# Kernel optimization log

Hardware: AMD Instinct MI355X
Metric: run time of the kernel (lower is better)

Reference implementation:

```python
import jax, jax.numpy as jnp
import numpy as np

B, N_REL, N_OBJ, N_ATT, VOCAB, D = 32, 1024, 1024, 4, 2048, 512


def setup_inputs() -> dict:
    key = jax.random.key(0)
    ks = jax.random.split(key, 12)
    inp = {}
    inp["ssg_rel"] = jax.random.randint(ks[0], (B, N_REL, 3), 0, N_OBJ, dtype=jnp.int32)
    inp["ssg_obj"] = jax.random.randint(ks[1], (B, N_OBJ), 0, VOCAB, dtype=jnp.int32)
    inp["ssg_att"] = jax.random.randint(ks[2], (B, N_OBJ, N_ATT), 0, VOCAB, dtype=jnp.int32)
    inp["emb_table"] = jax.random.normal(ks[3], (VOCAB, D), jnp.float32) * 0.02
    def lin(k, fan_in):
        return jax.random.normal(k, (fan_in, D), jnp.float32) * (1.0 / np.sqrt(fan_in))
    inp["W_sbj"] = lin(ks[4], 3 * D); inp["b_sbj"] = jnp.zeros((D,), jnp.float32)
    inp["W_obj"] = lin(ks[5], 3 * D); inp["b_obj"] = jnp.zeros((D,), jnp.float32)
    inp["W_rel"] = lin(ks[6], 3 * D); inp["b_rel"] = jnp.zeros((D,), jnp.float32)
    inp["W_o"] = lin(ks[7], D);      inp["b_o"] = jnp.zeros((D,), jnp.float32)
    inp["W_a"] = lin(ks[8], 2 * D);  inp["b_a"] = jnp.zeros((D,), jnp.float32)
    return inp


def reference(ssg_rel, ssg_obj, ssg_att, emb_table,
              W_sbj, b_sbj, W_obj, b_obj, W_rel, b_rel, W_o, b_o, W_a, b_a):
    # Dropout is identity in eval mode.
    Bq, N_rel, _ = ssg_rel.shape
    _, N_obj, N_att = ssg_att.shape
    d = emb_table.shape[1]

    rel_mask = (ssg_rel[:, :, 2] == 1)[..., None]      # [B, N_rel, 1], True = pad
    obj_mask = ssg_obj == 1                            # [B, N_obj]
    attr_mask = ssg_att == 1                           # [B, N_obj, N_att]

    rel_emb = emb_table[ssg_rel[:, :, 2]]              # [B, N_rel, d]
    obj_emb = emb_table[ssg_obj]                       # [B, N_obj, d]
    attr_emb = emb_table[ssg_att]                      # [B, N_obj, N_att, d]

    sbj_id = ssg_rel[:, :, 0]
    obj_id = ssg_rel[:, :, 1]
    gather = lambda ids: jnp.take_along_axis(obj_emb, ids[..., None], axis=1)  # [B,N_rel,d]
    sbj_g = gather(sbj_id)
    obj_g = gather(obj_id)

    zfill = lambda x: jnp.where(rel_mask, 0.0, x)
    # Sequential overwriting matches the original: rel_obj/rel_rel use the UPDATED sbj/obj feats.
    sbj_f = zfill(jax.nn.relu(jnp.concatenate([sbj_g, obj_g, rel_emb], -1) @ W_sbj + b_sbj))
    obj_f = zfill(jax.nn.relu(jnp.concatenate([sbj_f, obj_g, rel_emb], -1) @ W_obj + b_obj))
    rel_f = zfill(jax.nn.relu(jnp.concatenate([sbj_f, obj_f, rel_emb], -1) @ W_rel + b_rel))

    node = jnp.where(obj_mask[..., None], 0.0, jax.nn.relu(obj_emb @ W_o + b_o))  # [B,N_obj,d]

    att_in = jnp.concatenate(
        [jnp.broadcast_to(obj_emb[:, :, None, :], (Bq, N_obj, N_att, d)), attr_emb], -1)
    att_f = jnp.where(attr_mask[..., None], 0.0, jax.nn.relu(att_in @ W_a + b_a))  # [B,N_obj,N_att,d]

    bidx = jnp.arange(Bq)[:, None]
    node = node.at[bidx, sbj_id].add(sbj_f)
    node = node.at[bidx, obj_id].add(obj_f)

    # Original builds counts=ones(B, 2*N_rel, N_obj+1) then scatters 1s into it -> a no-op,
    # so counts.sum(dim=1) == 2*N_rel everywhere; the divisor is the constant 2*N_rel.
    rel_object_feat = node / jnp.asarray(2.0 * N_rel, node.dtype)

    att_sum = att_f.sum(axis=2)                        # [B, N_obj, d]
    att_cnt = jnp.sum(~attr_mask, axis=-1)             # [B, N_obj] number of valid attrs
    attr_zero = att_cnt == 0
    denom = jnp.maximum(att_cnt, 1).astype(att_sum.dtype)[..., None]
    att_feat = jnp.where(attr_zero[..., None], 0.0, att_sum / denom)

    ssg_feat = jnp.concatenate([rel_object_feat, rel_f, att_feat], axis=1)
    ssg_mask = jnp.concatenate([obj_mask, rel_mask[..., 0], attr_zero], axis=1)[:, None, None, :]
    return ssg_feat, ssg_mask
```

## Files before the change

### kernel.cpp

```cpp
#include <hip/hip_runtime.h>
#include <hip/hip_bf16.h>

typedef __attribute__((ext_vector_type(8))) short bf16x8;
typedef __attribute__((ext_vector_type(4))) float f32x4;

#define N_OBJ 1024
#define N_REL 1024
#define NB 32
#define D 512
#define VOCAB 2048
#define M_ROWS (NB * N_REL)
#define PRE_BLK (VOCAB * D)
#define WT_BLK (D * D)

__device__ __forceinline__ ushort f2bf(float f) {
    union { float f; unsigned u; } v; v.f = f;
    unsigned u = v.u;
    unsigned r = (u + 0x7FFFu + ((u >> 16) & 1u)) >> 16;
    return (ushort)r;
}
__device__ __forceinline__ float bf2f(ushort h) {
    union { unsigned u; float f; } v; v.u = ((unsigned)h) << 16;
    return v.f;
}

__device__ __forceinline__ void gload16(const ushort* g, const ushort* l) {
    __builtin_amdgcn_global_load_lds(
        (const __attribute__((address_space(1))) void*)(unsigned long long)(const void*)g,
        (__attribute__((address_space(3))) void*)(unsigned)(unsigned long long)(const void*)l,
        16, 0, 0);
}
__device__ __forceinline__ unsigned lds_off(const void* p) {
    return (unsigned)(unsigned long long)(const __attribute__((address_space(3))) void*)p;
}
__device__ __forceinline__ bf16x8 ds_read128(unsigned off) {
    bf16x8 r;
    asm volatile("ds_read_b128 %0, %1" : "=v"(r) : "v"(off));
    return r;
}

__device__ __forceinline__ void gemm0_body(
    int mt, int nt, int q, int tid,
    ushort* __restrict__ sA, ushort* __restrict__ sB,
    const ushort* __restrict__ A, const ushort* __restrict__ WT,
    ushort* __restrict__ PREB) {
    const int m0 = mt * 128;
    const int wtq[9] = {0, 1, 2, 4, 5, 8, 9, 10, 11};
    const ushort* BT0 = WT + (size_t)wtq[q] * WT_BLK + (size_t)nt * 128 * 512;
    ushort* PREq = PREB + (size_t)q * PRE_BLK;

    const int wave = tid >> 6;
    const int wm = wave >> 1, wn = wave & 1;
    const int lr = tid & 15, lk = (tid & 63) >> 4;

    f32x4 acc[4][4];
#pragma unroll
    for (int mi = 0; mi < 4; mi++)
#pragma unroll
        for (int ni = 0; ni < 4; ni++)
            acc[mi][ni] = (f32x4){0.f, 0.f, 0.f, 0.f};

    const ushort* Ag = A + (size_t)m0 * 512;
    const int srow = tid >> 3;
    const int scol = (tid & 7) * 8;

    for (int k0 = 0; k0 < 512; k0 += 64) {
        const ushort* As = Ag + (size_t)srow * 512 + k0 + scol;
        const ushort* Bs = BT0 + (size_t)srow * 512 + k0 + scol;
#pragma unroll
        for (int i = 0; i < 4; i++)
            gload16(As + (size_t)i * 32 * 512, &sA[i * 2048 + tid * 8]);
#pragma unroll
        for (int i = 0; i < 4; i++)
            gload16(Bs + (size_t)i * 32 * 512, &sB[i * 2048 + tid * 8]);
        __syncthreads();
#pragma unroll
        for (int ks = 0; ks < 2; ks++) {
            bf16x8 af[4], bfr[4];
#pragma unroll
            for (int mi = 0; mi < 4; mi++)
                af[mi] = *(const bf16x8*)&sA[(wm * 64 + mi * 16 + lr) * 64 + ks * 32 + lk * 8];
#pragma unroll
            for (int ni = 0; ni < 4; ni++)
                bfr[ni] = *(const bf16x8*)&sB[(wn * 64 + ni * 16 + lr) * 64 + ks * 32 + lk * 8];
#pragma unroll
            for (int mi = 0; mi < 4; mi++)
#pragma unroll
                for (int ni = 0; ni < 4; ni++)
                    acc[mi][ni] = __builtin_amdgcn_mfma_f32_16x16x32_bf16(af[mi], bfr[ni], acc[mi][ni], 0, 0, 0);
        }
        __syncthreads();
    }
#pragma unroll
    for (int mi = 0; mi < 4; mi++)
#pragma unroll
        for (int ni = 0; ni < 4; ni++) {
            int ch = nt * 128 + wn * 64 + ni * 16 + lr;
#pragma unroll
            for (int j = 0; j < 4; j++) {
                int R = m0 + wm * 64 + mi * 16 + lk * 4 + j;
                PREq[(size_t)R * 512 + ch] = f2bf(acc[mi][ni][j]);
            }
        }
}

template <int MODE>
__global__ __launch_bounds__(512, 2)
void k_gemm8(const ushort* __restrict__ A, const ushort* __restrict__ WT,
             const ushort* __restrict__ PREB,
             const int* __restrict__ ssg_rel, const int* __restrict__ ssg_obj,
             const float* __restrict__ bias,
             ushort* __restrict__ featbuf, float* __restrict__ out0,
             float* __restrict__ out1) {
    constexpr int KTOT = (MODE == 2) ? 1024 : 512;
    constexpr int NK = KTOT / 32;
    constexpr int LDA = 1024;
    __shared__ __attribute__((aligned(16))) ushort lds[4 * 2 * 256 * 32];

    const int tid = threadIdx.x;
    int x = blockIdx.x & 7, jj = blockIdx.x >> 3;
    const int mt = x * 16 + (jj >> 1), nt = jj & 1;
    const int m0 = mt * 256, n0 = nt * 256;

    const ushort* BT0 = WT + (size_t)((MODE == 1) ? 3 : 6) * WT_BLK + (size_t)n0 * 512;
    const ushort* BT1 = (MODE == 2) ? (WT + (size_t)7 * WT_BLK + (size_t)n0 * 512) : nullptr;

    const ushort* Ag = A + (size_t)m0 * LDA;
    const int srow = tid >> 2;
    const int scol = (tid & 3) * 8;

    const int wave = tid >> 6, lane = tid & 63;
    const int wm = wave >> 2, wn = wave & 3;
    const int lr = lane & 15, lk = lane >> 4;

    f32x4 acc[8][4];
#pragma unroll
    for (int mi = 0; mi < 8; mi++)
#pragma unroll
        for (int ni = 0; ni < 4; ni++)
            acc[mi][ni] = (f32x4){0.f, 0.f, 0.f, 0.f};

#define STAGE(KT) do {                                                          \
        int _b = (KT) & 3;                                                      \
        ushort* _dA = &lds[(_b * 2 + 0) * 8192];                                \
        ushort* _dB = &lds[(_b * 2 + 1) * 8192];                                \
        int _k0 = (KT) * 32;                                                    \
        const ushort* _Bb = (MODE == 2 && _k0 >= 512) ? (BT1 + (_k0 - 512))     \
                                                      : (BT0 + _k0);            \
        gload16(Ag + (size_t)(srow) * LDA + _k0 + scol, _dA + srow * 32 + scol);        \
        gload16(Ag + (size_t)(srow + 128) * LDA + _k0 + scol, _dA + (srow + 128) * 32 + scol); \
        gload16(_Bb + (size_t)(srow) * 512 + scol, _dB + srow * 32 + scol);             \
        gload16(_Bb + (size_t)(srow + 128) * 512 + scol, _dB + (srow + 128) * 32 + scol); \
    } while (0)

    STAGE(0); STAGE(1); STAGE(2);

    for (int kt = 0; kt < NK; ++kt) {
        if (kt + 3 < NK) {
            asm volatile("s_waitcnt vmcnt(8)\n\ts_barrier" ::: "memory");
            STAGE(kt + 3);
        } else if (kt + 3 == NK) {
            asm volatile("s_waitcnt vmcnt(8)\n\ts_barrier" ::: "memory");
        } else if (kt + 2 == NK) {
            asm volatile("s_waitcnt vmcnt(4)\n\ts_barrier" ::: "memory");
        } else {
            asm volatile("s_waitcnt vmcnt(0)\n\ts_barrier" ::: "memory");
        }
        {
            int buf = kt & 3;
            unsigned baseA = lds_off(&lds[(buf * 2 + 0) * 8192]) + (unsigned)(wm * 128) * 64 + lk * 16;
            unsigned baseB = lds_off(&lds[(buf * 2 + 1) * 8192]) + (unsigned)(wn * 64) * 64 + lk * 16;
            bf16x8 bfr[4], af[8];
#pragma unroll
            for (int ni = 0; ni < 4; ni++)
                bfr[ni] = ds_read128(baseB + (unsigned)(ni * 16 + lr) * 64);
#pragma unroll
            for (int mi = 0; mi < 8; mi++)
                af[mi] = ds_read128(baseA + (unsigned)(mi * 16 + lr) * 64);
            asm volatile("s_waitcnt lgkmcnt(0)" ::: "memory");
            __builtin_amdgcn_sched_barrier(0);
            __builtin_amdgcn_s_setprio(1);
#pragma unroll
            for (int mi = 0; mi < 8; mi++)
#pragma unroll
                for (int ni = 0; ni < 4; ni++)
                    acc[mi][ni] = __builtin_amdgcn_mfma_f32_16x16x32_bf16(af[mi], bfr[ni], acc[mi][ni], 0, 0, 0);
            __builtin_amdgcn_s_setprio(0);
        }
    }
#undef STAGE

    __syncthreads();
    int* sIo  = (int*)lds;
    int* sRid = sIo + 256;
    if (tid < 256) {
        int R = m0 + tid;
        int rid = ssg_rel[R * 3 + 2];
        sRid[tid] = rid;
        if (MODE == 1) sIo[tid] = ssg_obj[(R & ~(N_OBJ - 1)) + ssg_rel[R * 3 + 1]];
        if (MODE == 2 && nt == 0) {
            int b = R >> 10, rr = R & (N_REL - 1);
            out1[(size_t)b * 3072 + 1024 + rr] = (rid == 1) ? 1.0f : 0.0f;
        }
    }
    __syncthreads();

#pragma unroll
    for (int mi = 0; mi < 8; mi++) {
#pragma unroll
        for (int ni = 0; ni < 4; ni++) {
            int ch = n0 + wn * 64 + ni * 16 + lr;
#pragma unroll
            for (int j = 0; j < 4; j++) {
                int rl = wm * 128 + mi * 16 + lk * 4 + j;
                int R = m0 + rl;
                float v = acc[mi][ni][j];
                if (MODE == 1) {
                    int rid = sRid[rl];
                    int io = sIo[rl];
                    float t = v + bf2f(PREB[(size_t)3 * PRE_BLK + (size_t)io * 512 + ch])
                                + bf2f(PREB[(size_t)4 * PRE_BLK + (size_t)rid * 512 + ch])
                                + bias[ch];
                    t = fmaxf(t, 0.f);
                    if (rid == 1) t = 0.f;
                    featbuf[(size_t)R * 1024 + 512 + ch] = f2bf(t);
                } else {
                    int rid = sRid[rl];
                    float t = v + bf2f(PREB[(size_t)5 * PRE_BLK + (size_t)rid * 512 + ch])
                                + bias[ch];
                    t = fmaxf(t, 0.f);
                    if (rid == 1) t = 0.f;
                    int b = R >> 10, rr = R & (N_REL - 1);
                    out0[((size_t)(b * 3072 + 1024 + rr)) * 512 + ch] = t;
                }
            }
        }
    }
}

__global__ __launch_bounds__(256)
void k_setup(const float* __restrict__ E, ushort* __restrict__ EB,
             const float* __restrict__ Wsbj, const float* __restrict__ Wobj,
             const float* __restrict__ Wrel, const float* __restrict__ Wo,
             const float* __restrict__ Wa, ushort* __restrict__ WT,
             int* __restrict__ cnt) {
    int blk = blockIdx.x, tid = threadIdx.x;
    if (blk < 1024) {
        int i = blk * 256 + tid;
        float4 v = ((const float4*)E)[i];
        ushort4 o; o.x = f2bf(v.x); o.y = f2bf(v.y); o.z = f2bf(v.z); o.w = f2bf(v.w);
        ((ushort4*)EB)[i] = o;
    } else if (blk < 4096) {
        __shared__ float s[32][33];
        int bb = blk - 1024;
        int q = bb >> 8, rem = bb & 255;
        int bx = rem & 15, by = rem >> 4;
        const float* src; int ro;
        if (q < 3)       { src = Wsbj; ro = q * 512; }
        else if (q < 6)  { src = Wobj; ro = (q - 3) * 512; }
        else if (q < 9)  { src = Wrel; ro = (q - 6) * 512; }
        else if (q == 9) { src = Wo;   ro = 0; }
        else             { src = Wa;   ro = (q - 10) * 512; }
        int tx = tid & 31, ty = tid >> 5;
        int kbase = by * 32, nbase = bx * 32;
#pragma unroll
        for (int i = 0; i < 4; i++) {
            int k = kbase + ty + i * 8;
            s[ty + i * 8][tx] = src[(size_t)(ro + k) * 512 + nbase + tx];
        }
        __syncthreads();
        ushort* dst = WT + (size_t)q * WT_BLK;
#pragma unroll
        for (int i = 0; i < 4; i++) {
            int n = nbase + ty + i * 8;
            dst[(size_t)n * 512 + kbase + tx] = f2bf(s[tx][ty + i * 8]);
        }
    } else {
        cnt[(blk - 4096) * 256 + tid] = 0;
    }
}

__global__ void k_csr_count(const int* __restrict__ ssg_rel, int* __restrict__ cnt) {
    int r = blockIdx.x * 256 + threadIdx.x;
    int bb = r & ~(N_OBJ - 1);
    atomicAdd(&cnt[bb + ssg_rel[r * 3 + 0]], 1);
    atomicAdd(&cnt[bb + ssg_rel[r * 3 + 1]], 1);
}

__global__ __launch_bounds__(1024)
void k_csr_scan(const int* __restrict__ cnt, int* __restrict__ offs, int* __restrict__ cursor) {
    __shared__ int part[1024];
    int t = threadIdx.x;
    int base = t * 32;
    int local[32];
    int sum = 0;
#pragma unroll
    for (int i = 0; i < 32; i++) { local[i] = sum; sum += cnt[base + i]; }
    part[t] = sum;
    __syncthreads();
    for (int d = 1; d < 1024; d <<= 1) {
        int v = (t >= d) ? part[t - d] : 0;
        __syncthreads();
        part[t] += v;
        __syncthreads();
    }
    int excl = (t == 0) ? 0 : part[t - 1];
#pragma unroll
    for (int i = 0; i < 32; i++) {
        int o = excl + local[i];
        offs[base + i] = o;
        cursor[base + i] = o;
    }
    if (t == 1023) offs[32768] = part[1023];
}

__global__ __launch_bounds__(256)
void k_pre_fill(const ushort* __restrict__ EB, const ushort* __restrict__ WT,
                ushort* __restrict__ PREB, const int* __restrict__ ssg_rel,
                int* __restrict__ cursor, int* __restrict__ lists) {
    int blk = blockIdx.x, tid = threadIdx.x;
    if (blk < 576) {
        int q = blk >> 6, mt = (blk >> 2) & 15, nt = blk & 3;
        if ((q == 2 || q == 4 || q == 5) && mt >= 8) return;
        __shared__ __attribute__((aligned(16))) ushort sA[128 * 64];
        __shared__ __attribute__((aligned(16))) ushort sB[128 * 64];
        gemm0_body(mt, nt, q, tid, sA, sB, EB, WT, PREB);
    } else {
        int r = (blk - 576) * 256 + tid;
        int bb = r & ~(N_OBJ - 1);
        int p0 = atomicAdd(&cursor[bb + ssg_rel[r * 3 + 0]], 1);
        lists[p0] = r * 2;
        int p1 = atomicAdd(&cursor[bb + ssg_rel[r * 3 + 1]], 1);
        lists[p1] = r * 2 + 1;
    }
}

__global__ void k_sbj(const int* __restrict__ ssg_rel, const int* __restrict__ ssg_obj,
                      const ushort* __restrict__ PREB, const float* __restrict__ b_sbj,
                      ushort* __restrict__ featbuf) {
    int R = blockIdx.x * 2 + (threadIdx.x >> 7);
    int c4 = threadIdx.x & 127;
    int sid = ssg_rel[R * 3 + 0];
    int oid = ssg_rel[R * 3 + 1];
    int rid = ssg_rel[R * 3 + 2];
    int bb = R & ~(N_OBJ - 1);
    int is_ = ssg_obj[bb + sid];
    int io  = ssg_obj[bb + oid];
    ushort4 p1 = ((const ushort4*)(PREB + (size_t)is_ * 512))[c4];
    ushort4 p2 = ((const ushort4*)(PREB + (size_t)1 * PRE_BLK + (size_t)io * 512))[c4];
    ushort4 p3 = ((const ushort4*)(PREB + (size_t)2 * PRE_BLK + (size_t)rid * 512))[c4];
    float4 b  = ((const float4*)b_sbj)[c4];
    float4 v;
    v.x = fmaxf(bf2f(p1.x) + bf2f(p2.x) + bf2f(p3.x) + b.x, 0.f);
    v.y = fmaxf(bf2f(p1.y) + bf2f(p2.y) + bf2f(p3.y) + b.y, 0.f);
    v.z = fmaxf(bf2f(p1.z) + bf2f(p2.z) + bf2f(p3.z) + b.z, 0.f);
    v.w = fmaxf(bf2f(p1.w) + bf2f(p2.w) + bf2f(p3.w) + b.w, 0.f);
    if (rid == 1) { v.x = v.y = v.z = v.w = 0.f; }
    ushort4 o; o.x = f2bf(v.x); o.y = f2bf(v.y); o.z = f2bf(v.z); o.w = f2bf(v.w);
    *(ushort4*)&featbuf[(size_t)R * 1024 + c4 * 4] = o;
}

__global__ void k_objpass(const int* __restrict__ ssg_obj, const int* __restrict__ ssg_att,
                          const int* __restrict__ offs, const int* __restrict__ lists,
                          const ushort* __restrict__ feat, const ushort* __restrict__ PREB,
                          const float* __restrict__ b_o, const float* __restrict__ b_a,
                          float* __restrict__ out0, float* __restrict__ out1) {
    int Ro = blockIdx.x * 2 + (threadIdx.x >> 7);
    int c4 = threadIdx.x & 127;
    int iv = ssg_obj[Ro];
    int bq = Ro >> 10, o = Ro & (N_OBJ - 1);

    float4 bo4 = ((const float4*)b_o)[c4];
    ushort4 q6 = ((const ushort4*)(PREB + (size_t)6 * PRE_BLK + (size_t)iv * 512))[c4];
    float a0 = 0.f, a1 = 0.f, a2 = 0.f, a3 = 0.f;
    if (iv != 1) {
        a0 = fmaxf(bf2f(q6.x) + bo4.x, 0.f);
        a1 = fmaxf(bf2f(q6.y) + bo4.y, 0.f);
        a2 = fmaxf(bf2f(q6.z) + bo4.z, 0.f);
        a3 = fmaxf(bf2f(q6.w) + bo4.w, 0.f);
    }
    int s = offs[Ro], e = offs[Ro + 1];
    for (int i = s; i < e; ++i) {
        int ent = lists[i];
        ushort4 u = ((const ushort4*)(feat + (size_t)(ent >> 1) * 1024 + (ent & 1) * 512))[c4];
        a0 += bf2f(u.x); a1 += bf2f(u.y); a2 += bf2f(u.z); a3 += bf2f(u.w);
    }
    float4 r;
    r.x = a0 * (1.0f / 2048.0f); r.y = a1 * (1.0f / 2048.0f);
    r.z = a2 * (1.0f / 2048.0f); r.w = a3 * (1.0f / 2048.0f);
    ((float4*)out0)[((size_t)(bq * 3072 + o)) * 128 + c4] = r;

    int j0 = ssg_att[Ro * 4 + 0], j1 = ssg_att[Ro * 4 + 1];
    int j2 = ssg_att[Ro * 4 + 2], j3 = ssg_att[Ro * 4 + 3];
    float4 ba4 = ((const float4*)b_a)[c4];
    ushort4 q7 = ((const ushort4*)(PREB + (size_t)7 * PRE_BLK + (size_t)iv * 512))[c4];
    float bx = bf2f(q7.x) + ba4.x, by = bf2f(q7.y) + ba4.y;
    float bz = bf2f(q7.z) + ba4.z, bw = bf2f(q7.w) + ba4.w;
    int cnt = (j0 != 1) + (j1 != 1) + (j2 != 1) + (j3 != 1);
    float inv = cnt ? 1.0f / (float)cnt : 0.f;
    float sx = 0.f, sy = 0.f, sz = 0.f, sw = 0.f;
    const ushort* A2 = PREB + (size_t)8 * PRE_BLK;
#define ACC_ATT(J) if ((J) != 1) { \
        ushort4 a2 = ((const ushort4*)(A2 + (size_t)(J) * 512))[c4]; \
        sx += fmaxf(bx + bf2f(a2.x), 0.f); sy += fmaxf(by + bf2f(a2.y), 0.f); \
        sz += fmaxf(bz + bf2f(a2.z), 0.f); sw += fmaxf(bw + bf2f(a2.w), 0.f); }
    ACC_ATT(j0) ACC_ATT(j1) ACC_ATT(j2) ACC_ATT(j3)
#undef ACC_ATT
    float4 sv; sv.x = sx * inv; sv.y = sy * inv; sv.z = sz * inv; sv.w = sw * inv;
    ((float4*)out0)[((size_t)(bq * 3072 + 2048 + o)) * 128 + c4] = sv;

    if (c4 == 0) {
        out1[(size_t)bq * 3072 + o] = (iv == 1) ? 1.0f : 0.0f;
        out1[(size_t)bq * 3072 + 2048 + o] = (cnt == 0) ? 1.0f : 0.0f;
    }
}

extern "C" void kernel_launch(void* const* d_in, const int* in_sizes, int n_in,
                              void* d_out, int out_size, void* d_ws, size_t ws_size,
                              hipStream_t stream) {
    const int*   ssg_rel = (const int*)d_in[0];
    const int*   ssg_obj = (const int*)d_in[1];
    const int*   ssg_att = (const int*)d_in[2];
    const float* emb     = (const float*)d_in[3];
    const float* Wsbj    = (const float*)d_in[4];
    const float* bsbj    = (const float*)d_in[5];
    const float* Wobj    = (const float*)d_in[6];
    const float* bobj    = (const float*)d_in[7];
    const float* Wrel    = (const float*)d_in[8];
    const float* brel    = (const float*)d_in[9];
    const float* Wo      = (const float*)d_in[10];
    const float* bo      = (const float*)d_in[11];
    const float* Wa      = (const float*)d_in[12];
    const float* ba      = (const float*)d_in[13];

    float* out0 = (float*)d_out;
    float* out1 = out0 + (size_t)NB * 3072 * 512;

    char* w = (char*)d_ws;
    ushort* EB     = (ushort*)w; w += (size_t)VOCAB * D * 2;
    ushort* WT     = (ushort*)w; w += (size_t)12 * WT_BLK * 2;
    ushort* PREB   = (ushort*)w; w += (size_t)9 * PRE_BLK * 2;
    ushort* feat   = (ushort*)w; w += (size_t)M_ROWS * 1024 * 2;
    int*    cnt    = (int*)   w; w += (size_t)32768 * 4;
    int*    offs   = (int*)   w; w += (size_t)32769 * 4;
    int*    cursor = (int*)   w; w += (size_t)32768 * 4;
    int*    lists  = (int*)   w; w += (size_t)65536 * 4;

    k_setup<<<dim3(4224), dim3(256), 0, stream>>>(emb, EB, Wsbj, Wobj, Wrel, Wo, Wa, WT, cnt);
    k_csr_count<<<dim3(128), dim3(256), 0, stream>>>(ssg_rel, cnt);
    k_csr_scan<<<dim3(1), dim3(1024), 0, stream>>>(cnt, offs, cursor);
    k_pre_fill<<<dim3(704), dim3(256), 0, stream>>>(EB, WT, PREB, ssg_rel, cursor, lists);
    k_sbj<<<dim3(M_ROWS / 2), dim3(256), 0, stream>>>(ssg_rel, ssg_obj, PREB, bsbj, feat);
    k_gemm8<1><<<dim3(256), dim3(512), 0, stream>>>(feat, WT, PREB, ssg_rel, ssg_obj,
                                                    bobj, feat, nullptr, nullptr);
    k_gemm8<2><<<dim3(256), dim3(512), 0, stream>>>(feat, WT, PREB, ssg_rel, ssg_obj,
                                                    brel, nullptr, out0, out1);
    k_objpass<<<dim3(M_ROWS / 2), dim3(256), 0, stream>>>(ssg_obj, ssg_att, offs, lists,
                                                          feat, PREB, bo, ba, out0, out1);
}
```

Measured before the change: 202.4 us.

## Reuse pipelined 256x256 GEMM body for vocab precompute; move attribute pass earlier

The small 128x128 GEMM used to precompute the vocab-by-weight tables in k_pre_fill is replaced by a templated version of the larger 256x256, 512-thread pipelined MFMA body already used by the main GEMMs. The grid shrinks from 576 to 120 GEMM blocks plus the CSR-fill blocks. The attribute-averaging work moves from the final object pass into the subject-feature kernel as extra blocks, leaving a lighter node-pass kernel at the end. The aim is a faster precompute GEMM and a shorter tail kernel. The cost is fewer blocks for the precompute GEMM, which may underfill the GPU.

```diff
diff --git a/kernel.cpp b/kernel.cpp
--- a/kernel.cpp
+++ b/kernel.cpp
@@ -39,91 +39,34 @@
     return r;
 }
 
-__device__ __forceinline__ void gemm0_body(
-    int mt, int nt, int q, int tid,
-    ushort* __restrict__ sA, ushort* __restrict__ sB,
+template <int MODE>
+__device__ __forceinline__ void gemm8_body(
+    int mt, int nt, int q, int tid, ushort* lds,
     const ushort* __restrict__ A, const ushort* __restrict__ WT,
-    ushort* __restrict__ PREB) {
-    const int m0 = mt * 128;
-    const int wtq[9] = {0, 1, 2, 4, 5, 8, 9, 10, 11};
-    const ushort* BT0 = WT + (size_t)wtq[q] * WT_BLK + (size_t)nt * 128 * 512;
-    ushort* PREq = PREB + (size_t)q * PRE_BLK;
-
-    const int wave = tid >> 6;
-    const int wm = wave >> 1, wn = wave & 1;
-    const int lr = tid & 15, lk = (tid & 63) >> 4;
-
-    f32x4 acc[4][4];
-#pragma unroll
-    for (int mi = 0; mi < 4; mi++)
-#pragma unroll
-        for (int ni = 0; ni < 4; ni++)
-            acc[mi][ni] = (f32x4){0.f, 0.f, 0.f, 0.f};
-
-    const ushort* Ag = A + (size_t)m0 * 512;
-    const int srow = tid >> 3;
-    const int scol = (tid & 7) * 8;
-
-    for (int k0 = 0; k0 < 512; k0 += 64) {
-        const ushort* As = Ag + (size_t)srow * 512 + k0 + scol;
-        const ushort* Bs = BT0 + (size_t)srow * 512 + k0 + scol;
-#pragma unroll
-        for (int i = 0; i < 4; i++)
-            gload16(As + (size_t)i * 32 * 512, &sA[i * 2048 + tid * 8]);
-#pragma unroll
-        for (int i = 0; i < 4; i++)
-            gload16(Bs + (size_t)i * 32 * 512, &sB[i * 2048 + tid * 8]);
-        __syncthreads();
-#pragma unroll
-        for (int ks = 0; ks < 2; ks++) {
-            bf16x8 af[4], bfr[4];
-#pragma unroll
-            for (int mi = 0; mi < 4; mi++)
-                af[mi] = *(const bf16x8*)&sA[(wm * 64 + mi * 16 + lr) * 64 + ks * 32 + lk * 8];
-#pragma unroll
-            for (int ni = 0; ni < 4; ni++)
-                bfr[ni] = *(const bf16x8*)&sB[(wn * 64 + ni * 16 + lr) * 64 + ks * 32 + lk * 8];
-#pragma unroll
-            for (int mi = 0; mi < 4; mi++)
-#pragma unroll
-                for (int ni = 0; ni < 4; ni++)
-                    acc[mi][ni] = __builtin_amdgcn_mfma_f32_16x16x32_bf16(af[mi], bfr[ni], acc[mi][ni], 0, 0, 0);
-        }
-        __syncthreads();
-    }
-#pragma unroll
-    for (int mi = 0; mi < 4; mi++)
-#pragma unroll
-        for (int ni = 0; ni < 4; ni++) {
-            int ch = nt * 128 + wn * 64 + ni * 16 + lr;
-#pragma unroll
-            for (int j = 0; j < 4; j++) {
-                int R = m0 + wm * 64 + mi * 16 + lk * 4 + j;
-                PREq[(size_t)R * 512 + ch] = f2bf(acc[mi][ni][j]);
-            }
-        }
-}
-
-template <int MODE>
-__global__ __launch_bounds__(512, 2)
-void k_gemm8(const ushort* __restrict__ A, const ushort* __restrict__ WT,
-             const ushort* __restrict__ PREB,
-             const int* __restrict__ ssg_rel, const int* __restrict__ ssg_obj,
-             const float* __restrict__ bias,
-             ushort* __restrict__ featbuf, float* __restrict__ out0,
-             float* __restrict__ out1) {
+    ushort* __restrict__ PREB,
+    const int* __restrict__ ssg_rel, const int* __restrict__ ssg_obj,
+    const float* __restrict__ bias,
+    ushort* __restrict__ featbuf, float* __restrict__ out0,
+    float* __restrict__ out1) {
     constexpr int KTOT = (MODE == 2) ? 1024 : 512;
     constexpr int NK = KTOT / 32;
-    constexpr int LDA = 1024;
-    __shared__ __attribute__((aligned(16))) ushort lds[4 * 2 * 256 * 32];
-
-    const int tid = threadIdx.x;
-    int x = blockIdx.x & 7, jj = blockIdx.x >> 3;
-    const int mt = x * 16 + (jj >> 1), nt = jj & 1;
+    constexpr int LDA = (MODE == 0) ? 512 : 1024;
+
     const int m0 = mt * 256, n0 = nt * 256;
 
-    const ushort* BT0 = WT + (size_t)((MODE == 1) ? 3 : 6) * WT_BLK + (size_t)n0 * 512;
-    const ushort* BT1 = (MODE == 2) ? (WT + (size_t)7 * WT_BLK + (size_t)n0 * 512) : nullptr;
+    const ushort* BT0;
+    const ushort* BT1 = nullptr;
+    ushort* PREq = nullptr;
+    if (MODE == 0) {
+        const int wtq[9] = {0, 1, 2, 4, 5, 8, 9, 10, 11};
+        BT0 = WT + (size_t)wtq[q] * WT_BLK + (size_t)n0 * 512;
+        PREq = PREB + (size_t)q * PRE_BLK;
+    } else if (MODE == 1) {
+        BT0 = WT + (size_t)3 * WT_BLK + (size_t)n0 * 512;
+    } else {
+        BT0 = WT + (size_t)6 * WT_BLK + (size_t)n0 * 512;
+        BT1 = WT + (size_t)7 * WT_BLK + (size_t)n0 * 512;
+    }
 
     const ushort* Ag = A + (size_t)m0 * LDA;
     const int srow = tid >> 2;
@@ -189,6 +132,21 @@
         }
     }
 #undef STAGE
+
+    if (MODE == 0) {
+#pragma unroll
+        for (int mi = 0; mi < 8; mi++)
+#pragma unroll
+            for (int ni = 0; ni < 4; ni++) {
+                int ch = n0 + wn * 64 + ni * 16 + lr;
+#pragma unroll
+                for (int j = 0; j < 4; j++) {
+                    int R = m0 + wm * 128 + mi * 16 + lk * 4 + j;
+                    PREq[(size_t)R * 512 + ch] = f2bf(acc[mi][ni][j]);
+                }
+            }
+        return;
+    }
 
     __syncthreads();
     int* sIo  = (int*)lds;
@@ -314,19 +272,26 @@
     if (t == 1023) offs[32768] = part[1023];
 }
 
-__global__ __launch_bounds__(256)
+__global__ __launch_bounds__(512, 2)
 void k_pre_fill(const ushort* __restrict__ EB, const ushort* __restrict__ WT,
                 ushort* __restrict__ PREB, const int* __restrict__ ssg_rel,
                 int* __restrict__ cursor, int* __restrict__ lists) {
+    __shared__ __attribute__((aligned(16))) ushort lds[4 * 2 * 256 * 32];
     int blk = blockIdx.x, tid = threadIdx.x;
-    if (blk < 576) {
-        int q = blk >> 6, mt = (blk >> 2) & 15, nt = blk & 3;
-        if ((q == 2 || q == 4 || q == 5) && mt >= 8) return;
-        __shared__ __attribute__((aligned(16))) ushort sA[128 * 64];
-        __shared__ __attribute__((aligned(16))) ushort sB[128 * 64];
-        gemm0_body(mt, nt, q, tid, sA, sB, EB, WT, PREB);
+    if (blk < 120) {
+        int q, mt, nt;
+        if (blk < 96) {
+            const int qf[6] = {0, 1, 3, 6, 7, 8};
+            q = qf[blk >> 4]; mt = (blk & 15) >> 1; nt = blk & 1;
+        } else {
+            const int qh[3] = {2, 4, 5};
+            int b = blk - 96;
+            q = qh[b >> 3]; mt = (b & 7) >> 1; nt = b & 1;
+        }
+        gemm8_body<0>(mt, nt, q, tid, lds, EB, WT, PREB,
+                      nullptr, nullptr, nullptr, nullptr, nullptr, nullptr);
     } else {
-        int r = (blk - 576) * 256 + tid;
+        int r = (blk - 120) * 512 + tid;
         int bb = r & ~(N_OBJ - 1);
         int p0 = atomicAdd(&cursor[bb + ssg_rel[r * 3 + 0]], 1);
         lists[p0] = r * 2;
@@ -335,36 +300,83 @@
     }
 }
 
-__global__ void k_sbj(const int* __restrict__ ssg_rel, const int* __restrict__ ssg_obj,
-                      const ushort* __restrict__ PREB, const float* __restrict__ b_sbj,
-                      ushort* __restrict__ featbuf) {
-    int R = blockIdx.x * 2 + (threadIdx.x >> 7);
-    int c4 = threadIdx.x & 127;
-    int sid = ssg_rel[R * 3 + 0];
-    int oid = ssg_rel[R * 3 + 1];
-    int rid = ssg_rel[R * 3 + 2];
-    int bb = R & ~(N_OBJ - 1);
-    int is_ = ssg_obj[bb + sid];
-    int io  = ssg_obj[bb + oid];
-    ushort4 p1 = ((const ushort4*)(PREB + (size_t)is_ * 512))[c4];
-    ushort4 p2 = ((const ushort4*)(PREB + (size_t)1 * PRE_BLK + (size_t)io * 512))[c4];
-    ushort4 p3 = ((const ushort4*)(PREB + (size_t)2 * PRE_BLK + (size_t)rid * 512))[c4];
-    float4 b  = ((const float4*)b_sbj)[c4];
-    float4 v;
-    v.x = fmaxf(bf2f(p1.x) + bf2f(p2.x) + bf2f(p3.x) + b.x, 0.f);
-    v.y = fmaxf(bf2f(p1.y) + bf2f(p2.y) + bf2f(p3.y) + b.y, 0.f);
-    v.z = fmaxf(bf2f(p1.z) + bf2f(p2.z) + bf2f(p3.z) + b.z, 0.f);
-    v.w = fmaxf(bf2f(p1.w) + bf2f(p2.w) + bf2f(p3.w) + b.w, 0.f);
-    if (rid == 1) { v.x = v.y = v.z = v.w = 0.f; }
-    ushort4 o; o.x = f2bf(v.x); o.y = f2bf(v.y); o.z = f2bf(v.z); o.w = f2bf(v.w);
-    *(ushort4*)&featbuf[(size_t)R * 1024 + c4 * 4] = o;
-}
-
-__global__ void k_objpass(const int* __restrict__ ssg_obj, const int* __restrict__ ssg_att,
-                          const int* __restrict__ offs, const int* __restrict__ lists,
-                          const ushort* __restrict__ feat, const ushort* __restrict__ PREB,
-                          const float* __restrict__ b_o, const float* __restrict__ b_a,
+__global__ void k_sbj_att(const int* __restrict__ ssg_rel, const int* __restrict__ ssg_obj,
+                          const int* __restrict__ ssg_att,
+                          const ushort* __restrict__ PREB,
+                          const float* __restrict__ b_sbj, const float* __restrict__ b_a,
+                          ushort* __restrict__ featbuf,
                           float* __restrict__ out0, float* __restrict__ out1) {
+    int blk = blockIdx.x, tid = threadIdx.x;
+    if (blk < 16384) {
+        int R = blk * 2 + (tid >> 7);
+        int c4 = tid & 127;
+        int sid = ssg_rel[R * 3 + 0];
+        int oid = ssg_rel[R * 3 + 1];
+        int rid = ssg_rel[R * 3 + 2];
+        int bb = R & ~(N_OBJ - 1);
+        int is_ = ssg_obj[bb + sid];
+        int io  = ssg_obj[bb + oid];
+        ushort4 p1 = ((const ushort4*)(PREB + (size_t)is_ * 512))[c4];
+        ushort4 p2 = ((const ushort4*)(PREB + (size_t)1 * PRE_BLK + (size_t)io * 512))[c4];
+        ushort4 p3 = ((const ushort4*)(PREB + (size_t)2 * PRE_BLK + (size_t)rid * 512))[c4];
+        float4 b  = ((const float4*)b_sbj)[c4];
+        float4 v;
+        v.x = fmaxf(bf2f(p1.x) + bf2f(p2.x) + bf2f(p3.x) + b.x, 0.f);
+        v.y = fmaxf(bf2f(p1.y) + bf2f(p2.y) + bf2f(p3.y) + b.y, 0.f);
+        v.z = fmaxf(bf2f(p1.z) + bf2f(p2.z) + bf2f(p3.z) + b.z, 0.f);
+        v.w = fmaxf(bf2f(p1.w) + bf2f(p2.w) + bf2f(p3.w) + b.w, 0.f);
+        if (rid == 1) { v.x = v.y = v.z = v.w = 0.f; }
+        ushort4 o; o.x = f2bf(v.x); o.y = f2bf(v.y); o.z = f2bf(v.z); o.w = f2bf(v.w);
+        *(ushort4*)&featbuf[(size_t)R * 1024 + c4 * 4] = o;
+    } else {
+        int Ro = (blk - 16384) * 2 + (tid >> 7);
+        int c4 = tid & 127;
+        int iv = ssg_obj[Ro];
+        int bq = Ro >> 10, o = Ro & (N_OBJ - 1);
+        int4 jj = ((const int4*)ssg_att)[Ro];
+        int j0 = jj.x, j1 = jj.y, j2 = jj.z, j3 = jj.w;
+        float4 ba4 = ((const float4*)b_a)[c4];
+        ushort4 q7 = ((const ushort4*)(PREB + (size_t)7 * PRE_BLK + (size_t)iv * 512))[c4];
+        float bx = bf2f(q7.x) + ba4.x, by = bf2f(q7.y) + ba4.y;
+        float bz = bf2f(q7.z) + ba4.z, bw = bf2f(q7.w) + ba4.w;
+        int cnt = (j0 != 1) + (j1 != 1) + (j2 != 1) + (j3 != 1);
+        float inv = cnt ? 1.0f / (float)cnt : 0.f;
+        float sx = 0.f, sy = 0.f, sz = 0.f, sw = 0.f;
+        const ushort* A2 = PREB + (size_t)8 * PRE_BLK;
+#define ACC_ATT(J) if ((J) != 1) { \
+            ushort4 a2 = ((const ushort4*)(A2 + (size_t)(J) * 512))[c4]; \
+            sx += fmaxf(bx + bf2f(a2.x), 0.f); sy += fmaxf(by + bf2f(a2.y), 0.f); \
+            sz += fmaxf(bz + bf2f(a2.z), 0.f); sw += fmaxf(bw + bf2f(a2.w), 0.f); }
+        ACC_ATT(j0) ACC_ATT(j1) ACC_ATT(j2) ACC_ATT(j3)
+#undef ACC_ATT
+        float4 sv; sv.x = sx * inv; sv.y = sy * inv; sv.z = sz * inv; sv.w = sw * inv;
+        ((float4*)out0)[((size_t)(bq * 3072 + 2048 + o)) * 128 + c4] = sv;
+        if (c4 == 0) {
+            out1[(size_t)bq * 3072 + o] = (iv == 1) ? 1.0f : 0.0f;
+            out1[(size_t)bq * 3072 + 2048 + o] = (cnt == 0) ? 1.0f : 0.0f;
+        }
+    }
+}
+
+template <int MODE>
+__global__ __launch_bounds__(512, 2)
+void k_gemm8(const ushort* __restrict__ A, const ushort* __restrict__ WT,
+             ushort* __restrict__ PREB,
+             const int* __restrict__ ssg_rel, const int* __restrict__ ssg_obj,
+             const float* __restrict__ bias,
+             ushort* __restrict__ featbuf, float* __restrict__ out0,
+             float* __restrict__ out1) {
+    __shared__ __attribute__((aligned(16))) ushort lds[4 * 2 * 256 * 32];
+    int x = blockIdx.x & 7, jj = blockIdx.x >> 3;
+    int mt = x * 16 + (jj >> 1), nt = jj & 1;
+    gemm8_body<MODE>(mt, nt, 0, threadIdx.x, lds, A, WT, PREB,
+                     ssg_rel, ssg_obj, bias, featbuf, out0, out1);
+}
+
+__global__ void k_nodepass(const int* __restrict__ ssg_obj,
+                           const int* __restrict__ offs, const int* __restrict__ lists,
+                           const ushort* __restrict__ feat, const ushort* __restrict__ PREB,
+                           const float* __restrict__ b_o, float* __restrict__ out0) {
     int Ro = blockIdx.x * 2 + (threadIdx.x >> 7);
     int c4 = threadIdx.x & 127;
     int iv = ssg_obj[Ro];
@@ -389,30 +401,6 @@
     r.x = a0 * (1.0f / 2048.0f); r.y = a1 * (1.0f / 2048.0f);
     r.z = a2 * (1.0f / 2048.0f); r.w = a3 * (1.0f / 2048.0f);
     ((float4*)out0)[((size_t)(bq * 3072 + o)) * 128 + c4] = r;
-
-    int j0 = ssg_att[Ro * 4 + 0], j1 = ssg_att[Ro * 4 + 1];
-    int j2 = ssg_att[Ro * 4 + 2], j3 = ssg_att[Ro * 4 + 3];
-    float4 ba4 = ((const float4*)b_a)[c4];
-    ushort4 q7 = ((const ushort4*)(PREB + (size_t)7 * PRE_BLK + (size_t)iv * 512))[c4];
-    float bx = bf2f(q7.x) + ba4.x, by = bf2f(q7.y) + ba4.y;
-    float bz = bf2f(q7.z) + ba4.z, bw = bf2f(q7.w) + ba4.w;
-    int cnt = (j0 != 1) + (j1 != 1) + (j2 != 1) + (j3 != 1);
-    float inv = cnt ? 1.0f / (float)cnt : 0.f;
-    float sx = 0.f, sy = 0.f, sz = 0.f, sw = 0.f;
-    const ushort* A2 = PREB + (size_t)8 * PRE_BLK;
-#define ACC_ATT(J) if ((J) != 1) { \
-        ushort4 a2 = ((const ushort4*)(A2 + (size_t)(J) * 512))[c4]; \
-        sx += fmaxf(bx + bf2f(a2.x), 0.f); sy += fmaxf(by + bf2f(a2.y), 0.f); \
-        sz += fmaxf(bz + bf2f(a2.z), 0.f); sw += fmaxf(bw + bf2f(a2.w), 0.f); }
-    ACC_ATT(j0) ACC_ATT(j1) ACC_ATT(j2) ACC_ATT(j3)
-#undef ACC_ATT
-    float4 sv; sv.x = sx * inv; sv.y = sy * inv; sv.z = sz * inv; sv.w = sw * inv;
-    ((float4*)out0)[((size_t)(bq * 3072 + 2048 + o)) * 128 + c4] = sv;
-
-    if (c4 == 0) {
-        out1[(size_t)bq * 3072 + o] = (iv == 1) ? 1.0f : 0.0f;
-        out1[(size_t)bq * 3072 + 2048 + o] = (cnt == 0) ? 1.0f : 0.0f;
-    }
 }
 
 extern "C" void kernel_launch(void* const* d_in, const int* in_sizes, int n_in,
@@ -449,12 +437,13 @@
     k_setup<<<dim3(4224), dim3(256), 0, stream>>>(emb, EB, Wsbj, Wobj, Wrel, Wo, Wa, WT, cnt);
     k_csr_count<<<dim3(128), dim3(256), 0, stream>>>(ssg_rel, cnt);
     k_csr_scan<<<dim3(1), dim3(1024), 0, stream>>>(cnt, offs, cursor);
-    k_pre_fill<<<dim3(704), dim3(256), 0, stream>>>(EB, WT, PREB, ssg_rel, cursor, lists);
-    k_sbj<<<dim3(M_ROWS / 2), dim3(256), 0, stream>>>(ssg_rel, ssg_obj, PREB, bsbj, feat);
+    k_pre_fill<<<dim3(184), dim3(512), 0, stream>>>(EB, WT, PREB, ssg_rel, cursor, lists);
+    k_sbj_att<<<dim3(32768), dim3(256), 0, stream>>>(ssg_rel, ssg_obj, ssg_att, PREB,
+                                                     bsbj, ba, feat, out0, out1);
     k_gemm8<1><<<dim3(256), dim3(512), 0, stream>>>(feat, WT, PREB, ssg_rel, ssg_obj,
                                                     bobj, feat, nullptr, nullptr);
     k_gemm8<2><<<dim3(256), dim3(512), 0, stream>>>(feat, WT, PREB, ssg_rel, ssg_obj,
                                                     brel, nullptr, out0, out1);
-    k_objpass<<<dim3(M_ROWS / 2), dim3(256), 0, stream>>>(ssg_obj, ssg_att, offs, lists,
-                                                          feat, PREB, bo, ba, out0, out1);
-}
+    k_nodepass<<<dim3(M_ROWS / 2), dim3(256), 0, stream>>>(ssg_obj, offs, lists,
+                                                           feat, PREB, bo, out0);
+}
```

Result: slower. 206.6 us (+2.1%).
